# Performance work log

Measured on AMD Instinct MI355X. Metric: run time of the kernel, lower is better.

The kernel has to match this reference:

```python
import jax, jax.numpy as jnp
import numpy as np

N_NODES = 100000
N_EDGES = 3200000
N_FEAT = 16
N_GRAPHS = 1024


def setup_inputs() -> dict:
    key = jax.random.key(0)
    ks = jax.random.split(key, 12)
    x = jax.random.normal(ks[0], (N_NODES, N_FEAT), dtype=jnp.float32)
    edge_index = jax.random.randint(ks[1], (2, N_EDGES), 0, N_NODES, dtype=jnp.int32)
    batch = jnp.sort(jax.random.randint(ks[2], (N_NODES,), 0, N_GRAPHS, dtype=jnp.int32))
    def lin(k, fan_in, fan_out):
        s = 1.0 / np.sqrt(fan_in)
        return jax.random.uniform(k, (fan_in, fan_out), jnp.float32, -s, s)
    W1 = lin(ks[3], N_FEAT, 64); b1 = jnp.zeros((64,), jnp.float32)
    W2 = lin(ks[4], 64, 32);     b2 = jnp.zeros((32,), jnp.float32)
    fc1_W = lin(ks[5], 32, 16);  fc1_b = jnp.zeros((16,), jnp.float32)
    fc2_W = lin(ks[6], 16, 1);   fc2_b = jnp.zeros((1,), jnp.float32)
    return {"x": x, "edge_index": edge_index, "batch": batch,
            "W1": W1, "b1": b1, "W2": W2, "b2": b2,
            "fc1_W": fc1_W, "fc1_b": fc1_b, "fc2_W": fc2_W, "fc2_b": fc2_b}


def _gcn_conv(h, W, b, src, dst, norm, n_nodes):
    # h: [N, Fin] -> [N, Fout]; symmetric-normalized scatter-add (PyG GCNConv)
    h = h @ W
    msg = h[src] * norm[:, None]            # edge-wise gather + scale
    out = jax.ops.segment_sum(msg, dst, num_segments=n_nodes)
    return out + b


def reference(x, edge_index, batch, W1, b1, W2, b2, fc1_W, fc1_b, fc2_W, fc2_b):
    n_nodes = x.shape[0]
    # add self-loops
    loops = jnp.arange(n_nodes, dtype=edge_index.dtype)
    src = jnp.concatenate([edge_index[0], loops])
    dst = jnp.concatenate([edge_index[1], loops])
    deg = jax.ops.segment_sum(jnp.ones_like(dst, dtype=x.dtype), dst, num_segments=n_nodes)
    dinv = jnp.where(deg > 0, jax.lax.rsqrt(deg), 0.0)
    norm = dinv[src] * dinv[dst]

    h = jax.nn.relu(_gcn_conv(x, W1, b1, src, dst, norm, n_nodes))
    # dropout p=0.2 is identity at inference
    h = jax.nn.relu(_gcn_conv(h, W2, b2, src, dst, norm, n_nodes))

    # global mean pool over graphs
    sums = jax.ops.segment_sum(h, batch, num_segments=N_GRAPHS)
    cnts = jax.ops.segment_sum(jnp.ones((n_nodes,), h.dtype), batch, num_segments=N_GRAPHS)
    g = sums / jnp.maximum(cnts, 1.0)[:, None]

    g = jax.nn.relu(g @ fc1_W + fc1_b)
    # dropout p=0.5 is identity at inference
    out = g @ fc2_W + fc2_b
    return jax.nn.sigmoid(out)  # [N_GRAPHS, 1]
```

## Files before the change

### kernel.cpp

```cpp
#include <hip/hip_runtime.h>
#include <math.h>

#define NNODES  100000
#define NEDGES  3200000
#define NGRAPHS 1024
#define BNODES  196
#define NBUCK   ((NNODES + BNODES - 1) / BNODES)
#define SCAP    12288
#define CHUNK   4096
#define NCHUNKS ((NEDGES + CHUNK - 1) / CHUNK)

typedef int iv4 __attribute__((ext_vector_type(4)));
typedef float fv2 __attribute__((ext_vector_type(2)));

#if defined(__has_builtin)
#if __has_builtin(__builtin_amdgcn_cvt_pk_f32_fp8) && __has_builtin(__builtin_amdgcn_cvt_pk_fp8_f32)
#define HW_FP8 1
#endif
#endif

__device__ __forceinline__ unsigned bf16pair(float a, float b) {
    unsigned ua = __float_as_uint(a), ub = __float_as_uint(b);
    ua += 0x7fffu + ((ua >> 16) & 1u);
    ub += 0x7fffu + ((ub >> 16) & 1u);
    return (ua >> 16) | (ub & 0xffff0000u);
}
__device__ __forceinline__ float bflo(unsigned u) { return __uint_as_float(u << 16); }
__device__ __forceinline__ float bfhi(unsigned u) { return __uint_as_float(u & 0xffff0000u); }

__device__ __forceinline__ unsigned fp8_of(float v) {
    unsigned s = (__float_as_uint(v) >> 24) & 0x80u;
    float a = fminf(fabsf(v), 448.f);
    unsigned ub = __float_as_uint(a);
    unsigned lsb = (ub >> 20) & 1u;
    ub += 0x0007FFFFu + lsb;
    int em = (int)(ub >> 20) - (120 << 3);
    if (em < 1) return s;
    if (em > 0x7E) em = 0x7E;
    return s | (unsigned)em;
}
__device__ __forceinline__ float fp8_to_f(unsigned b) {
    unsigned em = b & 0x7Fu;
    unsigned s = (b & 0x80u) << 24;
    float f = __uint_as_float(s | ((em + 0x3C0u) << 20));
    return (em >= 8u) ? f : 0.f;
}
__device__ __forceinline__ unsigned fp8x4_pack(float a, float b, float c, float d) {
    a = fminf(fmaxf(a, -448.f), 448.f);
    b = fminf(fmaxf(b, -448.f), 448.f);
    c = fminf(fmaxf(c, -448.f), 448.f);
    d = fminf(fmaxf(d, -448.f), 448.f);
#ifdef HW_FP8
    int w = __builtin_amdgcn_cvt_pk_fp8_f32(a, b, 0, false);
    w = __builtin_amdgcn_cvt_pk_fp8_f32(c, d, w, true);
    return (unsigned)w;
#else
    return fp8_of(a) | (fp8_of(b) << 8) | (fp8_of(c) << 16) | (fp8_of(d) << 24);
#endif
}
__device__ __forceinline__ fv2 f8lo(unsigned w) {
#ifdef HW_FP8
    return __builtin_amdgcn_cvt_pk_f32_fp8((int)w, false);
#else
    fv2 t; t.x = fp8_to_f(w & 0xFFu); t.y = fp8_to_f((w >> 8) & 0xFFu); return t;
#endif
}
__device__ __forceinline__ fv2 f8hi(unsigned w) {
#ifdef HW_FP8
    return __builtin_amdgcn_cvt_pk_f32_fp8((int)w, true);
#else
    fv2 t; t.x = fp8_to_f((w >> 16) & 0xFFu); t.y = fp8_to_f(w >> 24); return t;
#endif
}


__global__ void zero4_kernel(int4* p, int nvec) {
    int i = blockIdx.x * blockDim.x + threadIdx.x;
    if (i < nvec) p[i] = make_int4(0, 0, 0, 0);
}


__global__ void binA_kernel(const int* __restrict__ src, const int* __restrict__ dst,
                            int* __restrict__ bucketCur, int* __restrict__ stage) {
    __shared__ int lcnt[NBUCK + 1];
    __shared__ int boff[NBUCK + 1];
    __shared__ int gbase[NBUCK + 1];
    __shared__ int cur[NBUCK + 1];
    __shared__ int ssum[256];
    __shared__ int packed[CHUNK];
    __shared__ unsigned short bof[CHUNK];
    int tid = threadIdx.x;
    int beg = blockIdx.x * CHUNK;
    int end = beg + CHUNK; if (end > NEDGES) end = NEDGES;
    int cnt = end - beg;

    for (int i = tid; i <= NBUCK; i += 256) lcnt[i] = 0;
    __syncthreads();

    int ent[16];
    int bk[16];
#pragma unroll
    for (int it = 0; it < 4; ++it) {
        int e0 = beg + tid * 4 + it * 1024;
        if (e0 < end) {
            iv4 d4 = __builtin_nontemporal_load((const iv4*)(dst + e0));
            iv4 s4 = __builtin_nontemporal_load((const iv4*)(src + e0));
            int b;
            b = d4.x / BNODES; ent[it*4+0] = s4.x | ((d4.x - b*BNODES) << 17); bk[it*4+0] = b; atomicAdd(&lcnt[b], 1);
            b = d4.y / BNODES; ent[it*4+1] = s4.y | ((d4.y - b*BNODES) << 17); bk[it*4+1] = b; atomicAdd(&lcnt[b], 1);
            b = d4.z / BNODES; ent[it*4+2] = s4.z | ((d4.z - b*BNODES) << 17); bk[it*4+2] = b; atomicAdd(&lcnt[b], 1);
            b = d4.w / BNODES; ent[it*4+3] = s4.w | ((d4.w - b*BNODES) << 17); bk[it*4+3] = b; atomicAdd(&lcnt[b], 1);
        } else {
            bk[it*4+0] = -1; bk[it*4+1] = -1; bk[it*4+2] = -1; bk[it*4+3] = -1;
            ent[it*4+0] = 0; ent[it*4+1] = 0; ent[it*4+2] = 0; ent[it*4+3] = 0;
        }
    }
    __syncthreads();

    int b0 = 2 * tid, b1 = 2 * tid + 1;
    int c0 = lcnt[b0];
    int c1 = (b1 < NBUCK) ? lcnt[b1] : 0;
    int sum = c0 + c1;
    ssum[tid] = sum;
    __syncthreads();
    for (int o = 1; o < 256; o <<= 1) {
        int t = (tid >= o) ? ssum[tid - o] : 0;
        __syncthreads();
        ssum[tid] += t;
        __syncthreads();
    }
    int excl = ssum[tid] - sum;
    boff[b0] = excl; cur[b0] = excl;
    if (b1 < NBUCK) { boff[b1] = excl + c0; cur[b1] = excl + c0; }
    if (c0 > 0) gbase[b0] = atomicAdd(&bucketCur[b0], c0);
    if (b1 < NBUCK && c1 > 0) gbase[b1] = atomicAdd(&bucketCur[b1], c1);
    __syncthreads();

#pragma unroll
    for (int k = 0; k < 16; ++k) {
        int b = bk[k];
        if (b >= 0) {
            int p = atomicAdd(&cur[b], 1);
            packed[p] = ent[k];
            bof[p] = (unsigned short)b;
        }
    }
    __syncthreads();

    for (int i = tid; i < cnt; i += 256) {
        int b = bof[i];
        int addr = b * SCAP + gbase[b] + (i - boff[b]);
        stage[addr] = packed[i];
    }
}


__global__ void scanE_kernel(const int* __restrict__ bucketCur, int* __restrict__ ebase) {
    int lane = threadIdx.x;
    int run = 0;
    for (int base = 0; base < NBUCK; base += 64) {
        int idx = base + lane;
        int own = (idx < NBUCK) ? bucketCur[idx] : 0;
        int v = own;
        for (int o = 1; o < 64; o <<= 1) {
            int t = __shfl_up(v, o, 64);
            if (lane >= o) v += t;
        }
        if (idx < NBUCK) ebase[idx] = run + v - own;
        run += __shfl(v, 63, 64);
    }
}


__global__ void binB_kernel(const int* __restrict__ bucketCur, const int* __restrict__ ebase,
                            const int* __restrict__ stage, const float2* __restrict__ x,
                            int* __restrict__ entries, int* __restrict__ rowptr,
                            int* __restrict__ rowend, float* __restrict__ dinv,
                            unsigned* __restrict__ xs) {
    __shared__ int s[256];
    __shared__ int ncur[256];
    __shared__ float ndinv[256];
    int b = blockIdx.x;
    int cntE = bucketCur[b];
    int eb = ebase[b];
    int nlo = b * BNODES;
    int nn = NNODES - nlo; if (nn > BNODES) nn = BNODES;
    int sb = b * SCAP;
    int tid = threadIdx.x;

    s[tid] = 0;
    __syncthreads();
    for (int e = tid; e < cntE; e += 256) {
        unsigned w = (unsigned)stage[sb + e];
        atomicAdd(&s[w >> 17], 1);
    }
    __syncthreads();
    int v = s[tid];
    for (int o = 1; o < 256; o <<= 1) {
        int t = (tid >= o) ? s[tid - o] : 0;
        __syncthreads();
        s[tid] += t;
        __syncthreads();
    }
    int excl = s[tid] - v;
    ncur[tid] = excl;
    if (tid < nn) {
        rowptr[nlo + tid] = eb + excl;
        rowend[nlo + tid] = eb + excl + v;
        float di = rsqrtf((float)(v + 1));
        dinv[nlo + tid] = di;
        ndinv[tid] = di;
    }
    __syncthreads();
    for (int i = tid; i < nn * 8; i += 256) {
        int node = i >> 3, w = i & 7;
        float2 v2 = x[(size_t)(nlo + node) * 8 + w];
        float di = ndinv[node];
        xs[(nlo + node) * 8 + w] = bf16pair(v2.x * di, v2.y * di);
    }
    for (int e = tid; e < cntE; e += 256) {
        unsigned w = (unsigned)stage[sb + e];
        int dl = w >> 17;
        int slot = atomicAdd(&ncur[dl], 1);
        entries[eb + slot] = (int)(w & 0x1FFFFu);
    }
}


__device__ __forceinline__ void acc_bf(unsigned u, fv2& a) {
    fv2 t; t.x = bflo(u); t.y = bfhi(u);
    a += t;
}
#define ACCX4(V) { acc_bf((V).x, acc0); acc_bf((V).y, acc1); acc_bf((V).z, acc2); acc_bf((V).w, acc3); }
#define QRED(a) { a.x += __shfl_xor(a.x, 2); a.y += __shfl_xor(a.y, 2); \
                  a.x += __shfl_xor(a.x, 4); a.y += __shfl_xor(a.y, 4); }

__global__ void __launch_bounds__(256) gatherX_kernel(const int* __restrict__ entries,
        const int* __restrict__ rowptr, const int* __restrict__ rowend,
        const float* __restrict__ dinv, const uint4* __restrict__ xsv,
        float4* __restrict__ agg) {
    int t = blockIdx.x * 256 + threadIdx.x;
    int n = t >> 3, lane = t & 7;
    int half = lane & 1, quad = lane >> 1;
    int beg = rowptr[n], end = rowend[n];
    fv2 acc0 = {0.f, 0.f}, acc1 = {0.f, 0.f}, acc2 = {0.f, 0.f}, acc3 = {0.f, 0.f};
    if (quad == 0) {
        uint4 sv = xsv[n * 2 + half];
        ACCX4(sv);
    }

    int nb = (end - beg) >> 4;
    const int* ep = entries + beg + (quad << 2);
    iv4 e = {0, 0, 0, 0};
    if (nb > 0) __builtin_memcpy(&e, ep, 16);
    for (int i = 1; i <= nb; ++i) {
        iv4 f = e;
        if (i < nb) __builtin_memcpy(&e, ep + (i << 4), 16);
        uint4 v0 = xsv[f.x * 2 + half];
        uint4 v1 = xsv[f.y * 2 + half];
        uint4 v2 = xsv[f.z * 2 + half];
        uint4 v3 = xsv[f.w * 2 + half];
        ACCX4(v0); ACCX4(v1); ACCX4(v2); ACCX4(v3);
    }
    int tp = beg + (nb << 4) + (quad << 2);
#pragma unroll
    for (int j = 0; j < 4; ++j) {
        if (tp + j < end) {
            int ee = entries[tp + j];
            uint4 v = xsv[ee * 2 + half];
            ACCX4(v);
        }
    }

    QRED(acc0); QRED(acc1); QRED(acc2); QRED(acc3);

    if (quad == 0) {
        float di = dinv[n];
        float4 o0, o1;
        o0.x = acc0.x * di; o0.y = acc0.y * di; o0.z = acc1.x * di; o0.w = acc1.y * di;
        o1.x = acc2.x * di; o1.y = acc2.y * di; o1.z = acc3.x * di; o1.w = acc3.y * di;
        agg[n * 4 + half * 2 + 0] = o0;
        agg[n * 4 + half * 2 + 1] = o1;
    }
}


__global__ void __launch_bounds__(256) mlp_kernel(const float4* __restrict__ agg,
        const float* __restrict__ dinv,
        const float* __restrict__ W1, const float* __restrict__ b1,
        const float* __restrict__ W2, unsigned* __restrict__ hm2f) {
    __shared__ __align__(16) float w1s[16 * 64];
    __shared__ __align__(16) float w2s[64 * 32];
    __shared__ float bb1[64];
    __shared__ __align__(16) float h1s[32][68];
    int tid = threadIdx.x;
    for (int i = tid; i < 16 * 64; i += 256) w1s[i] = W1[i];
    for (int i = tid; i < 64 * 32; i += 256) w2s[i] = W2[i];
    if (tid < 64) bb1[tid] = b1[tid];

    int nl = tid >> 3, lane = tid & 7;
    int n = blockIdx.x * 32 + nl;
    const float4* ag = agg + n * 4;
    float4 A0 = ag[0], A1 = ag[1], A2 = ag[2], A3 = ag[3];
    float a[16] = {A0.x, A0.y, A0.z, A0.w, A1.x, A1.y, A1.z, A1.w,
                   A2.x, A2.y, A2.z, A2.w, A3.x, A3.y, A3.z, A3.w};
    __syncthreads();

    {
        int j0 = lane * 8;
        float h[8];
#pragma unroll
        for (int jj = 0; jj < 8; ++jj) h[jj] = bb1[j0 + jj];
#pragma unroll
        for (int k = 0; k < 16; ++k) {
            const float4* wr = (const float4*)(w1s + k * 64 + j0);
            float4 wa = wr[0], wb = wr[1];
            float av = a[k];
            h[0] += av * wa.x; h[1] += av * wa.y; h[2] += av * wa.z; h[3] += av * wa.w;
            h[4] += av * wb.x; h[5] += av * wb.y; h[6] += av * wb.z; h[7] += av * wb.w;
        }
        float4 r0, r1;
        r0.x = fmaxf(h[0], 0.f); r0.y = fmaxf(h[1], 0.f); r0.z = fmaxf(h[2], 0.f); r0.w = fmaxf(h[3], 0.f);
        r1.x = fmaxf(h[4], 0.f); r1.y = fmaxf(h[5], 0.f); r1.z = fmaxf(h[6], 0.f); r1.w = fmaxf(h[7], 0.f);
        float4* hw = (float4*)(&h1s[nl][j0]);
        hw[0] = r0; hw[1] = r1;
    }
    __syncthreads();

    {
        int j0 = lane * 4;
        float c0 = 0.f, c1 = 0.f, c2 = 0.f, c3 = 0.f;
#pragma unroll
        for (int k = 0; k < 64; k += 4) {
            float4 hv = *(const float4*)(&h1s[nl][k]);
            float4 w0 = *(const float4*)(w2s + (k + 0) * 32 + j0);
            float4 w1v = *(const float4*)(w2s + (k + 1) * 32 + j0);
            float4 w2v = *(const float4*)(w2s + (k + 2) * 32 + j0);
            float4 w3 = *(const float4*)(w2s + (k + 3) * 32 + j0);
            c0 += hv.x * w0.x; c1 += hv.x * w0.y; c2 += hv.x * w0.z; c3 += hv.x * w0.w;
            c0 += hv.y * w1v.x; c1 += hv.y * w1v.y; c2 += hv.y * w1v.z; c3 += hv.y * w1v.w;
            c0 += hv.z * w2v.x; c1 += hv.z * w2v.y; c2 += hv.z * w2v.z; c3 += hv.z * w2v.w;
            c0 += hv.w * w3.x; c1 += hv.w * w3.y; c2 += hv.w * w3.z; c3 += hv.w * w3.w;
        }
        float sc = dinv[n] * 64.f;
        hm2f[n * 8 + lane] = fp8x4_pack(c0 * sc, c1 * sc, c2 * sc, c3 * sc);
    }
}


#define ACCH4(V) { q0lo += f8lo((V).x); q0hi += f8hi((V).x); \
                   q1lo += f8lo((V).y); q1hi += f8hi((V).y); \
                   q2lo += f8lo((V).z); q2hi += f8hi((V).z); \
                   q3lo += f8lo((V).w); q3hi += f8hi((V).w); }

__global__ void __launch_bounds__(256) gatherH_pool_kernel(const int* __restrict__ entries,
        const int* __restrict__ rowptr, const int* __restrict__ rowend,
        const float* __restrict__ dinv, const uint4* __restrict__ hm4,
        const float4* __restrict__ b2, const int* __restrict__ batch,
        float* __restrict__ psum, float* __restrict__ pcnt) {
    __shared__ float lps[8][32];
    __shared__ float lpc[8];
    int tid = threadIdx.x;
    ((float*)lps)[tid] = 0.f;
    if (tid < 8) lpc[tid] = 0.f;
    __syncthreads();

    int t = blockIdx.x * 256 + tid;
    int n = t >> 3, lane = t & 7;
    int half = lane & 1, quad = lane >> 1;
    int g0 = batch[blockIdx.x * 32];
    int beg = rowptr[n], end = rowend[n];
    fv2 q0lo = {0.f,0.f}, q0hi = {0.f,0.f}, q1lo = {0.f,0.f}, q1hi = {0.f,0.f},
        q2lo = {0.f,0.f}, q2hi = {0.f,0.f}, q3lo = {0.f,0.f}, q3hi = {0.f,0.f};
    if (quad == 0) {
        uint4 sv = hm4[n * 2 + half];
        ACCH4(sv);
    }

    int nb = (end - beg) >> 4;
    const int* ep = entries + beg + (quad << 2);
    iv4 e = {0, 0, 0, 0};
    if (nb > 0) __builtin_memcpy(&e, ep, 16);
    for (int i = 1; i <= nb; ++i) {
        iv4 f = e;
        if (i < nb) __builtin_memcpy(&e, ep + (i << 4), 16);
        uint4 v0 = hm4[f.x * 2 + half];
        uint4 v1 = hm4[f.y * 2 + half];
        uint4 v2 = hm4[f.z * 2 + half];
        uint4 v3 = hm4[f.w * 2 + half];
        ACCH4(v0); ACCH4(v1); ACCH4(v2); ACCH4(v3);
    }
    int tp = beg + (nb << 4) + (quad << 2);
#pragma unroll
    for (int j = 0; j < 4; ++j) {
        if (tp + j < end) {
            int ee = entries[tp + j];
            uint4 v = hm4[ee * 2 + half];
            ACCH4(v);
        }
    }

    QRED(q0lo); QRED(q0hi); QRED(q1lo); QRED(q1hi);
    QRED(q2lo); QRED(q2hi); QRED(q3lo); QRED(q3hi);

    if (quad == 0) {
        float sc = dinv[n] * (1.0f / 64.f);
        float4 bv0 = b2[half * 4 + 0], bv1 = b2[half * 4 + 1],
               bv2 = b2[half * 4 + 2], bv3 = b2[half * 4 + 3];
        float vv[16];
        vv[0]  = fmaxf(q0lo.x * sc + bv0.x, 0.f);
        vv[1]  = fmaxf(q0lo.y * sc + bv0.y, 0.f);
        vv[2]  = fmaxf(q0hi.x * sc + bv0.z, 0.f);
        vv[3]  = fmaxf(q0hi.y * sc + bv0.w, 0.f);
        vv[4]  = fmaxf(q1lo.x * sc + bv1.x, 0.f);
        vv[5]  = fmaxf(q1lo.y * sc + bv1.y, 0.f);
        vv[6]  = fmaxf(q1hi.x * sc + bv1.z, 0.f);
        vv[7]  = fmaxf(q1hi.y * sc + bv1.w, 0.f);
        vv[8]  = fmaxf(q2lo.x * sc + bv2.x, 0.f);
        vv[9]  = fmaxf(q2lo.y * sc + bv2.y, 0.f);
        vv[10] = fmaxf(q2hi.x * sc + bv2.z, 0.f);
        vv[11] = fmaxf(q2hi.y * sc + bv2.w, 0.f);
        vv[12] = fmaxf(q3lo.x * sc + bv3.x, 0.f);
        vv[13] = fmaxf(q3lo.y * sc + bv3.y, 0.f);
        vv[14] = fmaxf(q3hi.x * sc + bv3.z, 0.f);
        vv[15] = fmaxf(q3hi.y * sc + bv3.w, 0.f);

        int g = batch[n], gr = g - g0;
        if (gr < 8) {
            float* pg = &lps[gr][half * 16];
#pragma unroll
            for (int k2 = 0; k2 < 16; ++k2) atomicAdd(pg + k2, vv[k2]);
            if (lane == 0) atomicAdd(&lpc[gr], 1.0f);
        } else {
            float* pg = psum + g * 32 + half * 16;
#pragma unroll
            for (int k2 = 0; k2 < 16; ++k2) atomicAdd(pg + k2, vv[k2]);
            if (lane == 0) atomicAdd(&pcnt[g], 1.0f);
        }
    }
    __syncthreads();
    int grf = tid >> 5, f = tid & 31;
    float v = lps[grf][f];
    if (v != 0.f) atomicAdd(&psum[(g0 + grf) * 32 + f], v);
    if (f == 0) {
        float c = lpc[grf];
        if (c != 0.f) atomicAdd(&pcnt[g0 + grf], c);
    }
}


__global__ void head_kernel(const float* __restrict__ psum, const float* __restrict__ pcnt,
                            const float* __restrict__ fc1W, const float* __restrict__ fc1b,
                            const float* __restrict__ fc2W, const float* __restrict__ fc2b,
                            float* __restrict__ out) {
    int g = blockIdx.x * blockDim.x + threadIdx.x;
    if (g >= NGRAPHS) return;
    float inv = 1.0f / fmaxf(pcnt[g], 1.0f);
    float gv[32];
#pragma unroll
    for (int k = 0; k < 32; ++k) gv[k] = psum[g * 32 + k] * inv;
    float o = fc2b[0];
#pragma unroll
    for (int j = 0; j < 16; ++j) {
        float h = fc1b[j];
#pragma unroll
        for (int k = 0; k < 32; ++k) h += gv[k] * fc1W[k * 16 + j];
        h = fmaxf(h, 0.f);
        o += h * fc2W[j];
    }
    out[g] = 1.0f / (1.0f + expf(-o));
}


extern "C" void kernel_launch(void* const* d_in, const int* in_sizes, int n_in,
                              void* d_out, int out_size, void* d_ws, size_t ws_size,
                              hipStream_t stream) {
    const float* x    = (const float*)d_in[0];
    const int*   ei   = (const int*)d_in[1];
    const int*   batch= (const int*)d_in[2];
    const float* W1   = (const float*)d_in[3];
    const float* b1   = (const float*)d_in[4];
    const float* W2   = (const float*)d_in[5];
    const float* b2   = (const float*)d_in[6];
    const float* fc1W = (const float*)d_in[7];
    const float* fc1b = (const float*)d_in[8];
    const float* fc2W = (const float*)d_in[9];
    const float* fc2b = (const float*)d_in[10];
    float* out = (float*)d_out;

    const int* src = ei;
    const int* dst = ei + NEDGES;

    char* wsb = (char*)d_ws;
    int*      bucketCur = (int*)wsb;
    float*    psum      = (float*)(wsb + 2048);
    float*    pcnt      = (float*)(wsb + 133120);
    int*      ebase     = (int*)(wsb + 137216);
    float*    dinv      = (float*)(wsb + 139264);
    int*      rowptr    = (int*)(wsb + 539264);
    int*      rowend    = (int*)(wsb + 939264);
    int*      stage     = (int*)(wsb + 1339392);
    int*      entries   = (int*)(wsb + 26456064);
    unsigned* xs        = (unsigned*)(wsb + 39256064);
    unsigned* hm2f      = (unsigned*)(wsb + 42456064);
    float4*   agg       = (float4*)(wsb + 1339392);

    const int B = 256;
    zero4_kernel<<<(8576 + B - 1) / B, B, 0, stream>>>((int4*)wsb, 8576);

    binA_kernel<<<NCHUNKS, B, 0, stream>>>(src, dst, bucketCur, stage);
    scanE_kernel<<<1, 64, 0, stream>>>(bucketCur, ebase);
    binB_kernel<<<NBUCK, B, 0, stream>>>(bucketCur, ebase, stage, (const float2*)x,
                                         entries, rowptr, rowend, dinv, xs);

    const int GTH = NNODES * 8 / B;
    gatherX_kernel<<<GTH, B, 0, stream>>>(entries, rowptr, rowend, dinv,
                                          (const uint4*)xs, agg);
    mlp_kernel<<<NNODES / 32, B, 0, stream>>>((const float4*)agg, dinv, W1, b1, W2, hm2f);
    gatherH_pool_kernel<<<GTH, B, 0, stream>>>(entries, rowptr, rowend, dinv,
                                               (const uint4*)hm2f, (const float4*)b2,
                                               batch, psum, pcnt);
    head_kernel<<<(NGRAPHS + B - 1) / B, B, 0, stream>>>(psum, pcnt, fc1W, fc1b, fc2W, fc2b, out);
}
```

Measured before the change: 242.7 us.

## Replace two-pass bucketed CSR build with global histogram, scan, atomic scatter

Drops the local-memory bucketed binning (binA/scanE/binB with a staging buffer) and builds the CSR directly. It uses a global atomic histogram over dst, a three-kernel prefix scan that also computes dinv and the scaled bf16 x, and a scatter that claims each edge's slot with a global atomic on a per-row cursor. The goal is to cut the staging round-trip and the complex shared-memory work. In exchange it relies on 6.4M contended global atomics and random scattered 4-byte writes, which lose the locality the bucketed approach provided. Row order within a node becomes nondeterministic.

After: 519.6 us. +114.1%, slower.

```diff
diff --git a/kernel.cpp b/kernel.cpp
--- a/kernel.cpp
+++ b/kernel.cpp
@@ -4,11 +4,7 @@
 #define NNODES  100000
 #define NEDGES  3200000
 #define NGRAPHS 1024
-#define BNODES  196
-#define NBUCK   ((NNODES + BNODES - 1) / BNODES)
-#define SCAP    12288
-#define CHUNK   4096
-#define NCHUNKS ((NEDGES + CHUNK - 1) / CHUNK)
+#define SCANB   391
 
 typedef int iv4 __attribute__((ext_vector_type(4)));
 typedef float fv2 __attribute__((ext_vector_type(2)));
@@ -80,150 +76,94 @@
 }
 
 
-__global__ void binA_kernel(const int* __restrict__ src, const int* __restrict__ dst,
-                            int* __restrict__ bucketCur, int* __restrict__ stage) {
-    __shared__ int lcnt[NBUCK + 1];
-    __shared__ int boff[NBUCK + 1];
-    __shared__ int gbase[NBUCK + 1];
-    __shared__ int cur[NBUCK + 1];
-    __shared__ int ssum[256];
-    __shared__ int packed[CHUNK];
-    __shared__ unsigned short bof[CHUNK];
-    int tid = threadIdx.x;
-    int beg = blockIdx.x * CHUNK;
-    int end = beg + CHUNK; if (end > NEDGES) end = NEDGES;
-    int cnt = end - beg;
-
-    for (int i = tid; i <= NBUCK; i += 256) lcnt[i] = 0;
-    __syncthreads();
-
-    int ent[16];
-    int bk[16];
-#pragma unroll
-    for (int it = 0; it < 4; ++it) {
-        int e0 = beg + tid * 4 + it * 1024;
-        if (e0 < end) {
-            iv4 d4 = __builtin_nontemporal_load((const iv4*)(dst + e0));
-            iv4 s4 = __builtin_nontemporal_load((const iv4*)(src + e0));
-            int b;
-            b = d4.x / BNODES; ent[it*4+0] = s4.x | ((d4.x - b*BNODES) << 17); bk[it*4+0] = b; atomicAdd(&lcnt[b], 1);
-            b = d4.y / BNODES; ent[it*4+1] = s4.y | ((d4.y - b*BNODES) << 17); bk[it*4+1] = b; atomicAdd(&lcnt[b], 1);
-            b = d4.z / BNODES; ent[it*4+2] = s4.z | ((d4.z - b*BNODES) << 17); bk[it*4+2] = b; atomicAdd(&lcnt[b], 1);
-            b = d4.w / BNODES; ent[it*4+3] = s4.w | ((d4.w - b*BNODES) << 17); bk[it*4+3] = b; atomicAdd(&lcnt[b], 1);
-        } else {
-            bk[it*4+0] = -1; bk[it*4+1] = -1; bk[it*4+2] = -1; bk[it*4+3] = -1;
-            ent[it*4+0] = 0; ent[it*4+1] = 0; ent[it*4+2] = 0; ent[it*4+3] = 0;
-        }
-    }
-    __syncthreads();
-
-    int b0 = 2 * tid, b1 = 2 * tid + 1;
-    int c0 = lcnt[b0];
-    int c1 = (b1 < NBUCK) ? lcnt[b1] : 0;
-    int sum = c0 + c1;
-    ssum[tid] = sum;
-    __syncthreads();
-    for (int o = 1; o < 256; o <<= 1) {
-        int t = (tid >= o) ? ssum[tid - o] : 0;
-        __syncthreads();
-        ssum[tid] += t;
-        __syncthreads();
-    }
-    int excl = ssum[tid] - sum;
-    boff[b0] = excl; cur[b0] = excl;
-    if (b1 < NBUCK) { boff[b1] = excl + c0; cur[b1] = excl + c0; }
-    if (c0 > 0) gbase[b0] = atomicAdd(&bucketCur[b0], c0);
-    if (b1 < NBUCK && c1 > 0) gbase[b1] = atomicAdd(&bucketCur[b1], c1);
-    __syncthreads();
-
-#pragma unroll
-    for (int k = 0; k < 16; ++k) {
-        int b = bk[k];
-        if (b >= 0) {
-            int p = atomicAdd(&cur[b], 1);
-            packed[p] = ent[k];
-            bof[p] = (unsigned short)b;
-        }
-    }
-    __syncthreads();
-
-    for (int i = tid; i < cnt; i += 256) {
-        int b = bof[i];
-        int addr = b * SCAP + gbase[b] + (i - boff[b]);
-        stage[addr] = packed[i];
-    }
-}
-
-
-__global__ void scanE_kernel(const int* __restrict__ bucketCur, int* __restrict__ ebase) {
-    int lane = threadIdx.x;
-    int run = 0;
-    for (int base = 0; base < NBUCK; base += 64) {
-        int idx = base + lane;
-        int own = (idx < NBUCK) ? bucketCur[idx] : 0;
-        int v = own;
-        for (int o = 1; o < 64; o <<= 1) {
-            int t = __shfl_up(v, o, 64);
-            if (lane >= o) v += t;
-        }
-        if (idx < NBUCK) ebase[idx] = run + v - own;
-        run += __shfl(v, 63, 64);
-    }
-}
-
-
-__global__ void binB_kernel(const int* __restrict__ bucketCur, const int* __restrict__ ebase,
-                            const int* __restrict__ stage, const float2* __restrict__ x,
-                            int* __restrict__ entries, int* __restrict__ rowptr,
-                            int* __restrict__ rowend, float* __restrict__ dinv,
-                            unsigned* __restrict__ xs) {
+__global__ void __launch_bounds__(256) hist_kernel(const int* __restrict__ dst,
+                                                   int* __restrict__ rowcnt) {
+    int t = blockIdx.x * 256 + threadIdx.x;
+    iv4 d4 = __builtin_nontemporal_load((const iv4*)dst + t);
+    atomicAdd(&rowcnt[d4.x], 1);
+    atomicAdd(&rowcnt[d4.y], 1);
+    atomicAdd(&rowcnt[d4.z], 1);
+    atomicAdd(&rowcnt[d4.w], 1);
+}
+
+
+__global__ void __launch_bounds__(256) scanA_kernel(const int* __restrict__ rowcnt,
+        int* __restrict__ rowptr, int* __restrict__ part,
+        float* __restrict__ dinv, const float2* __restrict__ x, unsigned* __restrict__ xs) {
     __shared__ int s[256];
-    __shared__ int ncur[256];
-    __shared__ float ndinv[256];
-    int b = blockIdx.x;
-    int cntE = bucketCur[b];
-    int eb = ebase[b];
-    int nlo = b * BNODES;
-    int nn = NNODES - nlo; if (nn > BNODES) nn = BNODES;
-    int sb = b * SCAP;
-    int tid = threadIdx.x;
-
-    s[tid] = 0;
-    __syncthreads();
-    for (int e = tid; e < cntE; e += 256) {
-        unsigned w = (unsigned)stage[sb + e];
-        atomicAdd(&s[w >> 17], 1);
-    }
-    __syncthreads();
-    int v = s[tid];
+    __shared__ float nd[256];
+    int b = blockIdx.x, tid = threadIdx.x;
+    int i0 = b * 256, i = i0 + tid;
+    int c = (i < NNODES) ? rowcnt[i] : 0;
+    s[tid] = c;
+    __syncthreads();
     for (int o = 1; o < 256; o <<= 1) {
         int t = (tid >= o) ? s[tid - o] : 0;
         __syncthreads();
         s[tid] += t;
         __syncthreads();
     }
-    int excl = s[tid] - v;
-    ncur[tid] = excl;
-    if (tid < nn) {
-        rowptr[nlo + tid] = eb + excl;
-        rowend[nlo + tid] = eb + excl + v;
-        float di = rsqrtf((float)(v + 1));
-        dinv[nlo + tid] = di;
-        ndinv[tid] = di;
-    }
-    __syncthreads();
-    for (int i = tid; i < nn * 8; i += 256) {
-        int node = i >> 3, w = i & 7;
-        float2 v2 = x[(size_t)(nlo + node) * 8 + w];
-        float di = ndinv[node];
-        xs[(nlo + node) * 8 + w] = bf16pair(v2.x * di, v2.y * di);
-    }
-    for (int e = tid; e < cntE; e += 256) {
-        unsigned w = (unsigned)stage[sb + e];
-        int dl = w >> 17;
-        int slot = atomicAdd(&ncur[dl], 1);
-        entries[eb + slot] = (int)(w & 0x1FFFFu);
-    }
+    int excl = s[tid] - c;
+    if (i < NNODES) {
+        rowptr[i] = excl;
+        float di = rsqrtf((float)(c + 1));
+        dinv[i] = di;
+        nd[tid] = di;
+    }
+    if (tid == 255) part[b] = s[255];
+    __syncthreads();
+    int nn = NNODES - i0; if (nn > 256) nn = 256;
+    for (int k = tid; k < nn * 8; k += 256) {
+        int node = k >> 3, w = k & 7;
+        float2 v2 = x[(size_t)(i0 + node) * 8 + w];
+        float di = nd[node];
+        xs[(i0 + node) * 8 + w] = bf16pair(v2.x * di, v2.y * di);
+    }
+}
+
+
+__global__ void scanB_kernel(int* __restrict__ part) {
+    int lane = threadIdx.x;
+    int run = 0;
+    for (int base = 0; base < SCANB; base += 64) {
+        int idx = base + lane;
+        int own = (idx < SCANB) ? part[idx] : 0;
+        int v = own;
+        for (int o = 1; o < 64; o <<= 1) {
+            int t = __shfl_up(v, o, 64);
+            if (lane >= o) v += t;
+        }
+        if (idx < SCANB) part[idx] = run + v - own;
+        run += __shfl(v, 63, 64);
+    }
+}
+
+
+__global__ void __launch_bounds__(256) scanC_kernel(int* __restrict__ rowptr,
+        const int* __restrict__ part, int* __restrict__ cur) {
+    int i = blockIdx.x * 256 + threadIdx.x;
+    if (i < NNODES) {
+        int r = rowptr[i] + part[blockIdx.x];
+        rowptr[i] = r;
+        cur[i] = r;
+    }
+    if (i == 0) rowptr[NNODES] = NEDGES;
+}
+
+
+__global__ void __launch_bounds__(256) scatter_kernel(const int* __restrict__ src,
+        const int* __restrict__ dst, int* __restrict__ cur, int* __restrict__ entries) {
+    int t = blockIdx.x * 256 + threadIdx.x;
+    iv4 s4 = __builtin_nontemporal_load((const iv4*)src + t);
+    iv4 d4 = __builtin_nontemporal_load((const iv4*)dst + t);
+    int p0 = atomicAdd(&cur[d4.x], 1);
+    int p1 = atomicAdd(&cur[d4.y], 1);
+    int p2 = atomicAdd(&cur[d4.z], 1);
+    int p3 = atomicAdd(&cur[d4.w], 1);
+    entries[p0] = s4.x;
+    entries[p1] = s4.y;
+    entries[p2] = s4.z;
+    entries[p3] = s4.w;
 }
 
 
@@ -236,13 +176,13 @@
                   a.x += __shfl_xor(a.x, 4); a.y += __shfl_xor(a.y, 4); }
 
 __global__ void __launch_bounds__(256) gatherX_kernel(const int* __restrict__ entries,
-        const int* __restrict__ rowptr, const int* __restrict__ rowend,
+        const int* __restrict__ rowptr,
         const float* __restrict__ dinv, const uint4* __restrict__ xsv,
         float4* __restrict__ agg) {
     int t = blockIdx.x * 256 + threadIdx.x;
     int n = t >> 3, lane = t & 7;
     int half = lane & 1, quad = lane >> 1;
-    int beg = rowptr[n], end = rowend[n];
+    int beg = rowptr[n], end = rowptr[n + 1];
     fv2 acc0 = {0.f, 0.f}, acc1 = {0.f, 0.f}, acc2 = {0.f, 0.f}, acc3 = {0.f, 0.f};
     if (quad == 0) {
         uint4 sv = xsv[n * 2 + half];
@@ -354,7 +294,7 @@
                    q3lo += f8lo((V).w); q3hi += f8hi((V).w); }
 
 __global__ void __launch_bounds__(256) gatherH_pool_kernel(const int* __restrict__ entries,
-        const int* __restrict__ rowptr, const int* __restrict__ rowend,
+        const int* __restrict__ rowptr,
         const float* __restrict__ dinv, const uint4* __restrict__ hm4,
         const float4* __restrict__ b2, const int* __restrict__ batch,
         float* __restrict__ psum, float* __restrict__ pcnt) {
@@ -369,7 +309,7 @@
     int n = t >> 3, lane = t & 7;
     int half = lane & 1, quad = lane >> 1;
     int g0 = batch[blockIdx.x * 32];
-    int beg = rowptr[n], end = rowend[n];
+    int beg = rowptr[n], end = rowptr[n + 1];
     fv2 q0lo = {0.f,0.f}, q0hi = {0.f,0.f}, q1lo = {0.f,0.f}, q1hi = {0.f,0.f},
         q2lo = {0.f,0.f}, q2hi = {0.f,0.f}, q3lo = {0.f,0.f}, q3hi = {0.f,0.f};
     if (quad == 0) {
@@ -492,32 +432,33 @@
     const int* dst = ei + NEDGES;
 
     char* wsb = (char*)d_ws;
-    int*      bucketCur = (int*)wsb;
-    float*    psum      = (float*)(wsb + 2048);
-    float*    pcnt      = (float*)(wsb + 133120);
-    int*      ebase     = (int*)(wsb + 137216);
-    float*    dinv      = (float*)(wsb + 139264);
-    int*      rowptr    = (int*)(wsb + 539264);
-    int*      rowend    = (int*)(wsb + 939264);
-    int*      stage     = (int*)(wsb + 1339392);
-    int*      entries   = (int*)(wsb + 26456064);
-    unsigned* xs        = (unsigned*)(wsb + 39256064);
-    unsigned* hm2f      = (unsigned*)(wsb + 42456064);
-    float4*   agg       = (float4*)(wsb + 1339392);
+    int*      rowcnt  = (int*)wsb;
+    float*    psum    = (float*)(wsb + 400000);
+    float*    pcnt    = (float*)(wsb + 531072);
+    int*      part    = (int*)(wsb + 535168);
+    int*      rowptr  = (int*)(wsb + 536768);
+    int*      cur     = (int*)(wsb + 936784);
+    float*    dinv    = (float*)(wsb + 1336784);
+    unsigned* xs      = (unsigned*)(wsb + 1736784);
+    unsigned* hm2f    = (unsigned*)(wsb + 4936784);
+    int*      entries = (int*)(wsb + 8136784);
+    float4*   agg     = (float4*)(wsb + 20936784);
 
     const int B = 256;
-    zero4_kernel<<<(8576 + B - 1) / B, B, 0, stream>>>((int4*)wsb, 8576);
-
-    binA_kernel<<<NCHUNKS, B, 0, stream>>>(src, dst, bucketCur, stage);
-    scanE_kernel<<<1, 64, 0, stream>>>(bucketCur, ebase);
-    binB_kernel<<<NBUCK, B, 0, stream>>>(bucketCur, ebase, stage, (const float2*)x,
-                                         entries, rowptr, rowend, dinv, xs);
+    zero4_kernel<<<(33448 + B - 1) / B, B, 0, stream>>>((int4*)wsb, 33448);
+
+    hist_kernel<<<NEDGES / (B * 4), B, 0, stream>>>(dst, rowcnt);
+    scanA_kernel<<<SCANB, B, 0, stream>>>(rowcnt, rowptr, part, dinv,
+                                          (const float2*)x, xs);
+    scanB_kernel<<<1, 64, 0, stream>>>(part);
+    scanC_kernel<<<SCANB, B, 0, stream>>>(rowptr, part, cur);
+    scatter_kernel<<<NEDGES / (B * 4), B, 0, stream>>>(src, dst, cur, entries);
 
     const int GTH = NNODES * 8 / B;
-    gatherX_kernel<<<GTH, B, 0, stream>>>(entries, rowptr, rowend, dinv,
+    gatherX_kernel<<<GTH, B, 0, stream>>>(entries, rowptr, dinv,
                                           (const uint4*)xs, agg);
     mlp_kernel<<<NNODES / 32, B, 0, stream>>>((const float4*)agg, dinv, W1, b1, W2, hm2f);
-    gatherH_pool_kernel<<<GTH, B, 0, stream>>>(entries, rowptr, rowend, dinv,
+    gatherH_pool_kernel<<<GTH, B, 0, stream>>>(entries, rowptr, dinv,
                                                (const uint4*)hm2f, (const float4*)b2,
                                                batch, psum, pcnt);
     head_kernel<<<(NGRAPHS + B - 1) / B, B, 0, stream>>>(psum, pcnt, fc1W, fc1b, fc2W, fc2b, out);
```
